# Optimization experiments

Hardware: AMD Instinct MI355X
Metric: run time of the kernel (lower is better)

## Reference

```python
import jax, jax.numpy as jnp
import numpy as np

B, T, D, M = 4, 4096, 1024, 1024
EPS = 1e-6


def _rms_norm(x, w):
    return x * jax.lax.rsqrt(jnp.mean(x * x, axis=-1, keepdims=True) + EPS) * w


def _linrec(xg, r, h0):
    # h_t = x_t + r_t * h_{t-1}  (SRU-style linear recurrence, sqrll_kernel)
    def step(h, inp):
        xt, rt = inp
        h = xt + rt * h
        return h, h
    _, ys = jax.lax.scan(step, h0, (jnp.swapaxes(xg, 0, 1), jnp.swapaxes(r, 0, 1)))
    return jnp.swapaxes(ys, 0, 1)  # [B,T,M]


def setup_inputs() -> dict:
    key = jax.random.key(0)
    ks = jax.random.split(key, 16)
    s = 0.02
    return {
        "x": jax.random.normal(ks[0], (B, T, D), jnp.float32),
        "mem": jnp.zeros((B, M), jnp.float32),
        "norm_w": jnp.ones((D,), jnp.float32),
        "wr_w": jax.random.normal(ks[1], (M, D), jnp.float32) * s,
        "wr_b": jnp.zeros((M,), jnp.float32),
        "wi_w": jax.random.normal(ks[2], (M, D), jnp.float32) * s,
        "wig_w": jax.random.normal(ks[3], (M, D), jnp.float32) * s,
        "wig_b": jnp.zeros((M,), jnp.float32),
        "wog_w": jax.random.normal(ks[4], (M, D), jnp.float32) * s,
        "wog_b": jnp.zeros((M,), jnp.float32),
        "wo_w": jax.random.normal(ks[5], (D, M), jnp.float32) * s,
        "ffnorm_w": jnp.ones((D,), jnp.float32),
        "ffn_wi_w": jax.random.normal(ks[6], (M, D), jnp.float32) * s,
        "ffn_wg_w": jax.random.normal(ks[7], (M, D), jnp.float32) * s,
        "ffn_wg_b": jnp.zeros((M,), jnp.float32),
        "ffn_wo_w": jax.random.normal(ks[8], (D, M), jnp.float32) * s,
    }


def reference(x, mem, norm_w, wr_w, wr_b, wi_w, wig_w, wig_b, wog_w, wog_b,
              wo_w, ffnorm_w, ffn_wi_w, ffn_wg_w, ffn_wg_b, ffn_wo_w):
    # --- sqrll branch ---
    y = _rms_norm(x, norm_w)                                   # [B,T,D]
    ig = jax.nn.sigmoid(jnp.einsum('btd,md->btm', y, wig_w) + wig_b)
    og = jax.nn.sigmoid(jnp.einsum('btd,md->btm', y, wog_w) + wog_b)
    r = jax.nn.sigmoid(jnp.einsum('btd,md->btm', y, wr_w) + wr_b)
    xg = jnp.einsum('btd,md->btm', y, wi_w) * ig               # gated input
    h = _linrec(xg, r, mem)                                    # [B,T,M]
    mem_out = jax.lax.stop_gradient(h[:, -1])
    s = (h / (1.0 + jnp.abs(h))) * og                          # softsign * out gate
    x = x + jnp.einsum('btm,dm->btd', s, wo_w)                 # residual (dropout=0)
    # --- gated FFN branch ---
    z = _rms_norm(x, ffnorm_w)
    ff = jnp.einsum('btd,md->btm', z, ffn_wi_w) * jax.nn.sigmoid(
        jnp.einsum('btd,md->btm', z, ffn_wg_w) + ffn_wg_b)
    x = x + jnp.einsum('btm,dm->btd', ff, ffn_wo_w)
    return (x, mem_out)
```

## Files before the change

kernel.cpp:

```cpp
#include <hip/hip_runtime.h>
#include <stdint.h>


#define R_ROWS 16384
#define DIM    1024
#define MDIM   1024
#define TSEQ   4096
#define NCHUNK 64
#define TCH    64

typedef __attribute__((ext_vector_type(8))) short  bf16x8;
typedef __attribute__((ext_vector_type(8))) ushort u16x8;
typedef __attribute__((ext_vector_type(4))) float  f32x4;

__device__ __forceinline__ float bf2f(ushort u) {
  union { float f; unsigned int i; } x; x.i = ((unsigned int)u) << 16; return x.f;
}
__device__ __forceinline__ ushort f2bf(float f) {
  union { float f; unsigned int i; } x; x.f = f;
  unsigned int r = x.i + 0x7fffu + ((x.i >> 16) & 1u);
  return (ushort)(r >> 16);
}
__device__ __forceinline__ float sigmoidf_(float x) {
  return 1.0f / (1.0f + __expf(-x));
}
__device__ __forceinline__ void load_lds16(const void* g, void* s) {
  __builtin_amdgcn_global_load_lds(
      (const __attribute__((address_space(1))) void*)g,
      (__attribute__((address_space(3))) void*)s, 16, 0, 0);
}

__global__ __launch_bounds__(256)
void cvt_weights(const float* __restrict__ w0, const float* __restrict__ w1,
                 const float* __restrict__ w2, const float* __restrict__ w3,
                 const float* __restrict__ w4, const float* __restrict__ w5,
                 const float* __restrict__ w6, ushort* __restrict__ dst)
{
  const float* src;
  switch (blockIdx.y) {
    case 0: src = w0; break; case 1: src = w1; break;
    case 2: src = w2; break; case 3: src = w3; break;
    case 4: src = w4; break; case 5: src = w5; break;
    default: src = w6; break;
  }
  const int i = blockIdx.x * 256 + threadIdx.x;
  const size_t off = (size_t)blockIdx.y * 1048576 + (size_t)i * 4;
  const float4 v = *(const float4*)(src + (size_t)i * 4);
  ushort4 o; o.x = f2bf(v.x); o.y = f2bf(v.y); o.z = f2bf(v.z); o.w = f2bf(v.w);
  *(ushort4*)(dst + off) = o;
}

__global__ __launch_bounds__(256)
void cvt_one(const float* __restrict__ src, ushort* __restrict__ dst)
{
  const int i = blockIdx.x * 256 + threadIdx.x;
  const float4 v = *(const float4*)(src + (size_t)i * 4);
  ushort4 o; o.x = f2bf(v.x); o.y = f2bf(v.y); o.z = f2bf(v.z); o.w = f2bf(v.w);
  *(ushort4*)(dst + (size_t)i * 4) = o;
}

template<bool IN_F32>
__global__ __launch_bounds__(256)
void rmsnorm_k(const void* __restrict__ xin, const float* __restrict__ w,
               ushort* __restrict__ y)
{
  __shared__ float red[4];
  const int row = blockIdx.x;
  const int tid = threadIdx.x;
  const size_t base = (size_t)row * DIM + tid * 4;
  float v[4];
  if (IN_F32) {
    const float4 xv = *(const float4*)((const float*)xin + base);
    v[0] = xv.x; v[1] = xv.y; v[2] = xv.z; v[3] = xv.w;
  } else {
    const ushort4 xv = *(const ushort4*)((const ushort*)xin + base);
    v[0] = bf2f(xv.x); v[1] = bf2f(xv.y); v[2] = bf2f(xv.z); v[3] = bf2f(xv.w);
  }
  float ss = v[0]*v[0] + v[1]*v[1] + v[2]*v[2] + v[3]*v[3];
  for (int o = 32; o > 0; o >>= 1) ss += __shfl_down(ss, o, 64);
  const int wave = tid >> 6, lane = tid & 63;
  if (lane == 0) red[wave] = ss;
  __syncthreads();
  const float sum = red[0] + red[1] + red[2] + red[3];
  const float scale = rsqrtf(sum * (1.0f / DIM) + 1e-6f);
  const float4 wv = *(const float4*)(w + tid * 4);
  ushort4 o4;
  o4.x = f2bf(v[0] * scale * wv.x);
  o4.y = f2bf(v[1] * scale * wv.y);
  o4.z = f2bf(v[2] * scale * wv.z);
  o4.w = f2bf(v[3] * scale * wv.w);
  *(ushort4*)(y + base) = o4;
}

template<int MODE>
__global__ __launch_bounds__(512, 2)
void gemm8(const ushort* __restrict__ A, const ushort* __restrict__ W,
           const float* __restrict__ bias, const float* __restrict__ auxf,
           const ushort* __restrict__ auxb, ushort* __restrict__ outb,
           float* __restrict__ outf)
{
  __shared__ __align__(16) ushort lds[2][2][2][8192];
  const int tid  = threadIdx.x;
  const int bm = blockIdx.x, bn = blockIdx.y;
  const int wave = tid >> 6, lane = tid & 63;
  const int wm = wave >> 2, wn = wave & 3;
  const int quad = lane >> 4, l16 = lane & 15;
  const int axor = l16 & 7;

  const ushort* Ab = A + (size_t)bm * (256 * 1024);
  const ushort* Wb = W + (size_t)bn * (256 * 1024);

  f32x4 acc[8][4];
#pragma unroll
  for (int i = 0; i < 8; ++i)
#pragma unroll
    for (int j = 0; j < 4; ++j) acc[i][j] = (f32x4){0.f, 0.f, 0.f, 0.f};

  auto stage = [&](const ushort* __restrict__ base, int kt, int mat, int half) {
    ushort* dst = &lds[kt & 1][mat][half][0];
    const ushort* src = base + (size_t)half * (128 * 1024) + kt * 64;
#pragma unroll
    for (int q = 0; q < 2; ++q) {
      const int ci = q * 512 + tid;
      const int row = ci >> 3, c8 = ci & 7;
      load_lds16(src + (size_t)row * 1024 + ((c8 ^ (row & 7)) << 3),
                 dst + ci * 8);
    }
  };

  stage(Ab, 0, 0, 0); stage(Ab, 0, 0, 1);
  stage(Wb, 0, 1, 0); stage(Wb, 0, 1, 1);
  stage(Wb, 1, 1, 0); stage(Wb, 1, 1, 1);
  asm volatile("s_waitcnt vmcnt(4)" ::: "memory");
  __builtin_amdgcn_s_barrier();

  for (int ktc = 0; ktc < 16; ++ktc) {
    const int b = ktc & 1;
    const ushort* Ah = &lds[b][0][wm][0];
    const ushort* Bh = &lds[b][1][wn >> 1][0];
    const int brow0 = (wn & 1) * 64;
    bf16x8 bfr[4][2];
#pragma unroll
    for (int q = 0; q < 4; ++q) {
      if (q == 0) {
#pragma unroll
        for (int j = 0; j < 4; ++j)
#pragma unroll
          for (int ks = 0; ks < 2; ++ks)
            bfr[j][ks] = *(const bf16x8*)
                &Bh[(brow0 + j * 16 + l16) * 64 +
                    (((ks * 4 + quad) ^ axor) << 3)];
      }
      bf16x8 af[2][2];
#pragma unroll
      for (int p = 0; p < 2; ++p)
#pragma unroll
        for (int ks = 0; ks < 2; ++ks)
          af[p][ks] = *(const bf16x8*)
              &Ah[((2 * q + p) * 16 + l16) * 64 +
                  (((ks * 4 + quad) ^ axor) << 3)];
      if (q == 0 && ktc + 1 < 16) stage(Ab, ktc + 1, 0, 0);
      if (q == 1 && ktc + 1 < 16) stage(Ab, ktc + 1, 0, 1);
      if (q == 2 && ktc + 2 < 16) stage(Wb, ktc + 2, 1, 0);
      if (q == 3 && ktc + 2 < 16) stage(Wb, ktc + 2, 1, 1);
      __builtin_amdgcn_s_barrier();
      asm volatile("s_waitcnt lgkmcnt(0)" ::: "memory");
      __builtin_amdgcn_s_setprio(1);
#pragma unroll
      for (int p = 0; p < 2; ++p)
#pragma unroll
        for (int j = 0; j < 4; ++j)
#pragma unroll
          for (int ks = 0; ks < 2; ++ks)
            acc[2 * q + p][j] = __builtin_amdgcn_mfma_f32_16x16x32_bf16(
                af[p][ks], bfr[j][ks], acc[2 * q + p][j], 0, 0, 0);
      __builtin_amdgcn_s_setprio(0);
      if (q == 3) {
        if (ktc >= 14) asm volatile("s_waitcnt vmcnt(0)" ::: "memory");
        else           asm volatile("s_waitcnt vmcnt(4)" ::: "memory");
      }
      __builtin_amdgcn_s_barrier();
    }
  }

  const int rbase = bm * 256 + wm * 128 + quad * 4;
  const int cbase = bn * 256 + wn * 64 + l16;
#pragma unroll
  for (int j = 0; j < 4; ++j) {
    const int col = cbase + j * 16;
    const float bv = (MODE == 0) ? bias[col] : 0.f;
#pragma unroll
    for (int i = 0; i < 8; ++i) {
#pragma unroll
      for (int g = 0; g < 4; ++g) {
        const size_t idx = (size_t)(rbase + i * 16 + g) * 1024 + col;
        const float v = acc[i][j][g];
        if (MODE == 0)      outb[idx] = f2bf(sigmoidf_(v + bv));
        else if (MODE == 1) outb[idx] = f2bf(v + auxf[idx]);
        else if (MODE == 2) outb[idx] = f2bf(v * bf2f(auxb[idx]));
        else                outf[idx] = v + bf2f(auxb[idx]);
      }
    }
  }
}

__global__ __launch_bounds__(256)
void linrec_passA(ushort* __restrict__ xg, const ushort* __restrict__ r,
                  float* __restrict__ cL, float* __restrict__ cP)
{
  const int g = blockIdx.x * 256 + threadIdx.x;
  const int m = g & (MDIM - 1);
  const int bc = g >> 10;
  const int b = bc >> 6, c = bc & 63;
  const size_t base = ((size_t)(b * TSEQ + c * TCH)) * MDIM + m;
  float h = 0.f, p = 1.f;
  for (int t = 0; t < TCH; ++t) {
    const size_t idx = base + (size_t)t * MDIM;
    const float xv = bf2f(xg[idx]), rv = bf2f(r[idx]);
    h = fmaf(rv, h, xv);
    p *= rv;
    xg[idx] = f2bf(h);
  }
  cL[c * 4096 + b * MDIM + m] = h;
  cP[c * 4096 + b * MDIM + m] = p;
}

__global__ __launch_bounds__(256)
void linrec_passB(const float* __restrict__ cL, const float* __restrict__ cP,
                  const float* __restrict__ mem, float* __restrict__ cIn,
                  float* __restrict__ memout)
{
  const int g = blockIdx.x * 256 + threadIdx.x;
  float carry = mem[g];
  for (int c = 0; c < NCHUNK; ++c) {
    cIn[c * 4096 + g] = carry;
    carry = fmaf(cP[c * 4096 + g], carry, cL[c * 4096 + g]);
  }
  memout[g] = carry;
}

__global__ __launch_bounds__(256)
void linrec_passC(const ushort* __restrict__ L, const ushort* __restrict__ r,
                  const ushort* __restrict__ og, const float* __restrict__ cIn,
                  ushort* __restrict__ s)
{
  const int g = blockIdx.x * 256 + threadIdx.x;
  const int m = g & (MDIM - 1);
  const int bc = g >> 10;
  const int b = bc >> 6, c = bc & 63;
  const size_t base = ((size_t)(b * TSEQ + c * TCH)) * MDIM + m;
  const float cin = cIn[c * 4096 + b * MDIM + m];
  float p = 1.f;
  for (int t = 0; t < TCH; ++t) {
    const size_t idx = base + (size_t)t * MDIM;
    p *= bf2f(r[idx]);
    const float h = fmaf(p, cin, bf2f(L[idx]));
    const float sv = h / (1.0f + fabsf(h)) * bf2f(og[idx]);
    s[idx] = f2bf(sv);
  }
}

extern "C" void kernel_launch(void* const* d_in, const int* in_sizes, int n_in,
                              void* d_out, int out_size, void* d_ws, size_t ws_size,
                              hipStream_t stream)
{
  const float* x        = (const float*)d_in[0];
  const float* mem      = (const float*)d_in[1];
  const float* norm_w   = (const float*)d_in[2];
  const float* wr_w     = (const float*)d_in[3];
  const float* wr_b     = (const float*)d_in[4];
  const float* wi_w     = (const float*)d_in[5];
  const float* wig_w    = (const float*)d_in[6];
  const float* wig_b    = (const float*)d_in[7];
  const float* wog_w    = (const float*)d_in[8];
  const float* wog_b    = (const float*)d_in[9];
  const float* wo_w     = (const float*)d_in[10];
  const float* ffnorm_w = (const float*)d_in[11];
  const float* ffn_wi_w = (const float*)d_in[12];
  const float* ffn_wg_w = (const float*)d_in[13];
  const float* ffn_wg_b = (const float*)d_in[14];
  const float* ffn_wo_w = (const float*)d_in[15];
  float* outF = (float*)d_out;

  ushort* xgL  = (ushort*)d_out;
  ushort* wbf  = (ushort*)((char*)d_out + 33554432ULL);
  float*  memoutF = outF + 16777216;

  char* ws = (char*)d_ws;
  ushort* y   = (ushort*)(ws);
  ushort* r   = (ushort*)(ws + 33554432ULL);
  ushort* og  = (ushort*)(ws + 67108864ULL);
  float*  cL  = (float*) (ws + 100663296ULL);
  float*  cP  = (float*) (ws + 101711872ULL);
  float*  cIn = (float*) (ws + 102760448ULL);
  ushort* s   = y;
  ushort* x1  = og;
  ushort* z   = r;
  ushort* gf  = y;
  ushort* fwo_bf = (ushort*)(ws + 100663296ULL);

  ushort* wr_bf   = wbf + 0 * 1048576;
  ushort* wog_bf  = wbf + 1 * 1048576;
  ushort* wi_bf   = wbf + 2 * 1048576;
  ushort* wig_bf  = wbf + 3 * 1048576;
  ushort* wo_bf   = wbf + 4 * 1048576;
  ushort* fwi_bf  = wbf + 5 * 1048576;
  ushort* fwg_bf  = wbf + 6 * 1048576;

  const dim3 g8(64, 4);

  cvt_weights<<<dim3(1024, 7), 256, 0, stream>>>(
      wr_w, wog_w, wi_w, wig_w, wo_w, ffn_wi_w, ffn_wg_w, wbf);

  rmsnorm_k<true><<<R_ROWS, 256, 0, stream>>>(x, norm_w, y);
  gemm8<0><<<g8, 512, 0, stream>>>(y, wr_bf,  wr_b,  nullptr, nullptr, r,   nullptr);
  gemm8<0><<<g8, 512, 0, stream>>>(y, wog_bf, wog_b, nullptr, nullptr, og,  nullptr);
  gemm8<0><<<g8, 512, 0, stream>>>(y, wig_bf, wig_b, nullptr, nullptr, xgL, nullptr);
  gemm8<2><<<g8, 512, 0, stream>>>(y, wi_bf,  nullptr, nullptr, xgL, xgL, nullptr);
  linrec_passA<<<1024, 256, 0, stream>>>(xgL, r, cL, cP);
  linrec_passB<<<16, 256, 0, stream>>>(cL, cP, mem, cIn, memoutF);
  linrec_passC<<<1024, 256, 0, stream>>>(xgL, r, og, cIn, s);
  cvt_one<<<1024, 256, 0, stream>>>(ffn_wo_w, fwo_bf);
  gemm8<1><<<g8, 512, 0, stream>>>(s, wo_bf, nullptr, x, nullptr, x1, nullptr);
  rmsnorm_k<false><<<R_ROWS, 256, 0, stream>>>(x1, ffnorm_w, z);
  gemm8<0><<<g8, 512, 0, stream>>>(z, fwg_bf, ffn_wg_b, nullptr, nullptr, gf, nullptr);
  gemm8<2><<<g8, 512, 0, stream>>>(z, fwi_bf, nullptr, nullptr, gf, gf, nullptr);
  gemm8<3><<<g8, 512, 0, stream>>>(gf, fwo_bf, nullptr, nullptr, x1, nullptr, outF);
}
```

Measured before the change: 641.1 us.

## Stage GEMM epilogue through LDS for vector stores; vectorize linrec passes

The GEMM epilogue now writes accumulators into swizzled LDS in two halves, then reads them back row-contiguously so each thread emits float4-loaded, ushort4/float4-stored global accesses instead of scattered scalar 2-byte stores. The linrec scan passes A and C now process four adjacent channels per thread with 8-byte loads and stores and a quarter of the blocks. The aim is to cut uncoalesced, narrow memory transactions in the store-heavy epilogues and scan kernels. In exchange it adds barriers and LDS traffic at the end of each GEMM, and the scan kernels now launch only 256 blocks, which lowers parallelism for latency hiding.

```diff
diff --git a/kernel.cpp b/kernel.cpp
--- a/kernel.cpp
+++ b/kernel.cpp
@@ -183,24 +183,61 @@
     }
   }
 
-  const int rbase = bm * 256 + wm * 128 + quad * 4;
-  const int cbase = bn * 256 + wn * 64 + l16;
-#pragma unroll
-  for (int j = 0; j < 4; ++j) {
-    const int col = cbase + j * 16;
-    const float bv = (MODE == 0) ? bias[col] : 0.f;
-#pragma unroll
-    for (int i = 0; i < 8; ++i) {
-#pragma unroll
-      for (int g = 0; g < 4; ++g) {
-        const size_t idx = (size_t)(rbase + i * 16 + g) * 1024 + col;
-        const float v = acc[i][j][g];
-        if (MODE == 0)      outb[idx] = f2bf(sigmoidf_(v + bv));
-        else if (MODE == 1) outb[idx] = f2bf(v + auxf[idx]);
-        else if (MODE == 2) outb[idx] = f2bf(v * bf2f(auxb[idx]));
-        else                outf[idx] = v + bf2f(auxb[idx]);
+  float* C = (float*)&lds[0][0][0][0];
+#pragma unroll 1
+  for (int h = 0; h < 2; ++h) {
+    if (wm == h) {
+      const int cb = wn * 64;
+#pragma unroll
+      for (int i = 0; i < 8; ++i)
+#pragma unroll
+        for (int j = 0; j < 4; ++j)
+#pragma unroll
+          for (int g = 0; g < 4; ++g) {
+            const int rw = i * 16 + quad * 4 + g;
+            const int cw = cb + j * 16 + l16;
+            C[rw * 256 + (cw ^ (((rw >> 2) & 1) << 4))] = acc[i][j][g];
+          }
+    }
+    __syncthreads();
+#pragma unroll 1
+    for (int sp = 0; sp < 16; ++sp) {
+      const int lin = sp * 2048 + tid * 4;
+      const int row = lin >> 8, c4 = lin & 255;
+      const int xr = ((row >> 2) & 1) << 4;
+      const float4 v4 = *(const float4*)&C[row * 256 + (c4 ^ xr)];
+      const int rg = bm * 256 + h * 128 + row;
+      const int cg = bn * 256 + c4;
+      const size_t gidx = (size_t)rg * 1024 + cg;
+      if (MODE == 0) {
+        const float4 bv = *(const float4*)(bias + cg);
+        ushort4 o;
+        o.x = f2bf(sigmoidf_(v4.x + bv.x));
+        o.y = f2bf(sigmoidf_(v4.y + bv.y));
+        o.z = f2bf(sigmoidf_(v4.z + bv.z));
+        o.w = f2bf(sigmoidf_(v4.w + bv.w));
+        *(ushort4*)(outb + gidx) = o;
+      } else if (MODE == 1) {
+        const float4 a4 = *(const float4*)(auxf + gidx);
+        ushort4 o;
+        o.x = f2bf(v4.x + a4.x); o.y = f2bf(v4.y + a4.y);
+        o.z = f2bf(v4.z + a4.z); o.w = f2bf(v4.w + a4.w);
+        *(ushort4*)(outb + gidx) = o;
+      } else if (MODE == 2) {
+        const ushort4 a4 = *(const ushort4*)(auxb + gidx);
+        ushort4 o;
+        o.x = f2bf(v4.x * bf2f(a4.x)); o.y = f2bf(v4.y * bf2f(a4.y));
+        o.z = f2bf(v4.z * bf2f(a4.z)); o.w = f2bf(v4.w * bf2f(a4.w));
+        *(ushort4*)(outb + gidx) = o;
+      } else {
+        const ushort4 a4 = *(const ushort4*)(auxb + gidx);
+        float4 o;
+        o.x = v4.x + bf2f(a4.x); o.y = v4.y + bf2f(a4.y);
+        o.z = v4.z + bf2f(a4.z); o.w = v4.w + bf2f(a4.w);
+        *(float4*)(outf + gidx) = o;
       }
     }
+    __syncthreads();
   }
 }
 
@@ -209,20 +246,29 @@
                   float* __restrict__ cL, float* __restrict__ cP)
 {
   const int g = blockIdx.x * 256 + threadIdx.x;
-  const int m = g & (MDIM - 1);
-  const int bc = g >> 10;
+  const int m4 = (g & 255) << 2;
+  const int bc = g >> 8;
   const int b = bc >> 6, c = bc & 63;
-  const size_t base = ((size_t)(b * TSEQ + c * TCH)) * MDIM + m;
-  float h = 0.f, p = 1.f;
+  const size_t base = ((size_t)(b * TSEQ + c * TCH)) * MDIM + m4;
+  float h0 = 0.f, h1 = 0.f, h2 = 0.f, h3 = 0.f;
+  float p0 = 1.f, p1 = 1.f, p2 = 1.f, p3 = 1.f;
   for (int t = 0; t < TCH; ++t) {
     const size_t idx = base + (size_t)t * MDIM;
-    const float xv = bf2f(xg[idx]), rv = bf2f(r[idx]);
-    h = fmaf(rv, h, xv);
-    p *= rv;
-    xg[idx] = f2bf(h);
-  }
-  cL[c * 4096 + b * MDIM + m] = h;
-  cP[c * 4096 + b * MDIM + m] = p;
+    const ushort4 xv = *(const ushort4*)&xg[idx];
+    const ushort4 rv = *(const ushort4*)&r[idx];
+    const float r0 = bf2f(rv.x), r1 = bf2f(rv.y), r2 = bf2f(rv.z), r3 = bf2f(rv.w);
+    h0 = fmaf(r0, h0, bf2f(xv.x)); p0 *= r0;
+    h1 = fmaf(r1, h1, bf2f(xv.y)); p1 *= r1;
+    h2 = fmaf(r2, h2, bf2f(xv.z)); p2 *= r2;
+    h3 = fmaf(r3, h3, bf2f(xv.w)); p3 *= r3;
+    ushort4 o; o.x = f2bf(h0); o.y = f2bf(h1); o.z = f2bf(h2); o.w = f2bf(h3);
+    *(ushort4*)&xg[idx] = o;
+  }
+  const size_t cb = (size_t)c * 4096 + b * MDIM + m4;
+  float4 L4; L4.x = h0; L4.y = h1; L4.z = h2; L4.w = h3;
+  float4 P4; P4.x = p0; P4.y = p1; P4.z = p2; P4.w = p3;
+  *(float4*)&cL[cb] = L4;
+  *(float4*)&cP[cb] = P4;
 }
 
 __global__ __launch_bounds__(256)
@@ -245,18 +291,29 @@
                   ushort* __restrict__ s)
 {
   const int g = blockIdx.x * 256 + threadIdx.x;
-  const int m = g & (MDIM - 1);
-  const int bc = g >> 10;
+  const int m4 = (g & 255) << 2;
+  const int bc = g >> 8;
   const int b = bc >> 6, c = bc & 63;
-  const size_t base = ((size_t)(b * TSEQ + c * TCH)) * MDIM + m;
-  const float cin = cIn[c * 4096 + b * MDIM + m];
-  float p = 1.f;
+  const size_t base = ((size_t)(b * TSEQ + c * TCH)) * MDIM + m4;
+  const size_t cb = (size_t)c * 4096 + b * MDIM + m4;
+  const float4 ci = *(const float4*)&cIn[cb];
+  float p0 = 1.f, p1 = 1.f, p2 = 1.f, p3 = 1.f;
   for (int t = 0; t < TCH; ++t) {
     const size_t idx = base + (size_t)t * MDIM;
-    p *= bf2f(r[idx]);
-    const float h = fmaf(p, cin, bf2f(L[idx]));
-    const float sv = h / (1.0f + fabsf(h)) * bf2f(og[idx]);
-    s[idx] = f2bf(sv);
+    const ushort4 rv = *(const ushort4*)&r[idx];
+    const ushort4 lv = *(const ushort4*)&L[idx];
+    const ushort4 ov = *(const ushort4*)&og[idx];
+    p0 *= bf2f(rv.x); p1 *= bf2f(rv.y); p2 *= bf2f(rv.z); p3 *= bf2f(rv.w);
+    const float a0 = fmaf(p0, ci.x, bf2f(lv.x));
+    const float a1 = fmaf(p1, ci.y, bf2f(lv.y));
+    const float a2 = fmaf(p2, ci.z, bf2f(lv.z));
+    const float a3 = fmaf(p3, ci.w, bf2f(lv.w));
+    ushort4 o;
+    o.x = f2bf(a0 / (1.0f + fabsf(a0)) * bf2f(ov.x));
+    o.y = f2bf(a1 / (1.0f + fabsf(a1)) * bf2f(ov.y));
+    o.z = f2bf(a2 / (1.0f + fabsf(a2)) * bf2f(ov.z));
+    o.w = f2bf(a3 / (1.0f + fabsf(a3)) * bf2f(ov.w));
+    *(ushort4*)&s[idx] = o;
   }
 }
 
@@ -317,9 +374,9 @@
   gemm8<0><<<g8, 512, 0, stream>>>(y, wog_bf, wog_b, nullptr, nullptr, og,  nullptr);
   gemm8<0><<<g8, 512, 0, stream>>>(y, wig_bf, wig_b, nullptr, nullptr, xgL, nullptr);
   gemm8<2><<<g8, 512, 0, stream>>>(y, wi_bf,  nullptr, nullptr, xgL, xgL, nullptr);
-  linrec_passA<<<1024, 256, 0, stream>>>(xgL, r, cL, cP);
+  linrec_passA<<<256, 256, 0, stream>>>(xgL, r, cL, cP);
   linrec_passB<<<16, 256, 0, stream>>>(cL, cP, mem, cIn, memoutF);
-  linrec_passC<<<1024, 256, 0, stream>>>(xgL, r, og, cIn, s);
+  linrec_passC<<<256, 256, 0, stream>>>(xgL, r, og, cIn, s);
   cvt_one<<<1024, 256, 0, stream>>>(ffn_wo_w, fwo_bf);
   gemm8<1><<<g8, 512, 0, stream>>>(s, wo_bf, nullptr, x, nullptr, x1, nullptr);
   rmsnorm_k<false><<<R_ROWS, 256, 0, stream>>>(x1, ffnorm_w, z);
```

New measurement: 569.5 us. 1.13x faster.
